# Kernel optimization log

Measured on AMD Instinct MI355X. Metric: run time of the kernel, lower is better.

## Reference

```python
import jax, jax.numpy as jnp
import numpy as np

THRESHOLD = 0.5
NEG_POS = 3
ALPHA = 1.0


def cxcy_to_xy(b):
    return jnp.concatenate([b[:, :2] - b[:, 2:] / 2, b[:, :2] + b[:, 2:] / 2], axis=-1)


def xy_to_cxcy(b):
    return jnp.concatenate([(b[:, :2] + b[:, 2:]) / 2, b[:, 2:] - b[:, :2]], axis=-1)


def encode_bboxes(cxcy, priors_cxcy):
    # standard SSD encoding with variances (0.1, 0.2)
    g_cxcy = (cxcy[:, :2] - priors_cxcy[:, :2]) / (priors_cxcy[:, 2:] / 10.0)
    g_wh = jnp.log(cxcy[:, 2:] / priors_cxcy[:, 2:]) * 5.0
    return jnp.concatenate([g_cxcy, g_wh], axis=-1)


def compute_iou(a, b):
    # a: [n,4] xyxy, b: [m,4] xyxy -> [n,m]
    lt = jnp.maximum(a[:, None, :2], b[None, :, :2])
    rb = jnp.minimum(a[:, None, 2:], b[None, :, 2:])
    wh = jnp.clip(rb - lt, 0.0)
    inter = wh[..., 0] * wh[..., 1]
    area_a = (a[:, 2] - a[:, 0]) * (a[:, 3] - a[:, 1])
    area_b = (b[:, 2] - b[:, 0]) * (b[:, 3] - b[:, 1])
    return inter / (area_a[:, None] + area_b[None, :] - inter)


def setup_inputs() -> dict:
    key = jax.random.key(0)
    k1, k2, k3, k4, k5, k6 = jax.random.split(key, 6)
    B, D, C, O = 128, 8732, 21, 16
    loc_pred = jax.random.normal(k1, (B, D, 4), dtype=jnp.float32)
    cls_pred = jax.random.normal(k2, (B, D, C), dtype=jnp.float32)
    # valid gt boxes: xmin<xmax, ymin<ymax
    p = jax.random.uniform(k3, (B, O, 4), dtype=jnp.float32)
    x1 = jnp.minimum(p[..., 0], p[..., 2])
    x2 = jnp.maximum(p[..., 0], p[..., 2]) + 1e-2
    y1 = jnp.minimum(p[..., 1], p[..., 3])
    y2 = jnp.maximum(p[..., 1], p[..., 3]) + 1e-2
    gt_boxes = jnp.stack([x1, y1, x2, y2], axis=-1)
    gt_labels = jax.random.randint(k4, (B, O), 1, C)
    # priors in cxcywh, w/h in (0.05, 0.5)
    cxy = jax.random.uniform(k5, (D, 2), dtype=jnp.float32)
    wh = jax.random.uniform(k6, (D, 2), dtype=jnp.float32) * 0.45 + 0.05
    default_boxes = jnp.concatenate([cxy, wh], axis=-1)
    return {"loc_pred": loc_pred, "cls_pred": cls_pred, "gt_boxes": gt_boxes,
            "gt_labels": gt_labels, "default_boxes": default_boxes}


def _match_and_losses(loc_pred, cls_pred, gt_boxes, gt_labels, default_boxes):
    B, D, C = cls_pred.shape
    O = gt_boxes.shape[1]
    db_xy = cxcy_to_xy(default_boxes)

    def match_one(boxes_i, labels_i):
        iou = compute_iou(boxes_i, db_xy)                 # [O, D]
        best_truth_overlap = iou.max(axis=0)              # [D]
        best_truth_idx = iou.argmax(axis=0)               # [D]
        best_default_idx = iou.argmax(axis=1)             # [O]
        best_truth_idx = best_truth_idx.at[best_default_idx].set(jnp.arange(O))
        best_truth_overlap = best_truth_overlap.at[best_default_idx].set(1.0)
        labels = labels_i[best_truth_idx]                 # [D]
        labels = jnp.where(best_truth_overlap < THRESHOLD, 0, labels)
        matched_xy = boxes_i[best_truth_idx]              # [D,4]
        loc = encode_bboxes(xy_to_cxcy(matched_xy), default_boxes)
        return loc, labels

    loc_t, conf_t = jax.vmap(match_one)(gt_boxes, gt_labels)  # [B,D,4], [B,D]
    loc_t = jax.lax.stop_gradient(loc_t)  # targets carry no grad (requires_grad=False)

    pos = conf_t > 0                                      # [B,D]
    n_positive = pos.sum(axis=1)                          # [B]
    n_pos_total = n_positive.sum()

    # SmoothL1 (beta=1), mean over positive elements (num_pos * 4)
    diff = loc_pred - loc_t
    ad = jnp.abs(diff)
    sl1 = jnp.where(ad < 1.0, 0.5 * diff * diff, ad - 0.5)
    loc_loss = (sl1 * pos[..., None]).sum() / (n_pos_total.astype(jnp.float32) * 4.0)

    # per-element cross entropy
    logp = jax.nn.log_softmax(cls_pred, axis=-1)          # [B,D,C]
    ce = -jnp.take_along_axis(logp, conf_t[..., None], axis=-1)[..., 0]  # [B,D]

    conf_pos_sum = (ce * pos).sum()
    neg_loss = jnp.where(pos, 0.0, ce)
    neg_sorted = -jnp.sort(-neg_loss, axis=1)             # descending per row
    ranks = jnp.arange(D)[None, :]
    hard = ranks < (NEG_POS * n_positive)[:, None]
    conf_neg_sum = (neg_sorted * hard).sum()
    conf_loss = (conf_neg_sum + conf_pos_sum) / n_pos_total.astype(jnp.float32)

    return ALPHA * loc_loss + conf_loss


def reference(loc_pred, cls_pred, gt_boxes, gt_labels, default_boxes):
    return _match_and_losses(loc_pred, cls_pred, gt_boxes, gt_labels, default_boxes)
```

## Files before the change

### kernel.cpp

```cpp
#include <hip/hip_runtime.h>

#define BB 128
#define DD 8732
#define OO 16
#define CC 21
#define CH 16
#define CHUNK 546
#define NBLK_D 35
#define NLB (BB * NBLK_D)
#define NV 35

typedef __attribute__((address_space(3))) unsigned int lds_u32;
typedef const __attribute__((address_space(1))) unsigned int glb_u32;

__device__ __forceinline__ float smoothl1(float d) {
    float ad = fabsf(d);
    return (ad < 1.0f) ? 0.5f * d * d : ad - 0.5f;
}

__global__ __launch_bounds__(256) void match_a(
    const float4* __restrict__ gt_boxes,
    const float4* __restrict__ db,
    unsigned long long* __restrict__ partial,
    unsigned* __restrict__ bpk,
    int* __restrict__ done_counter)
{
    const int b = blockIdx.y, ch = blockIdx.x, tid = threadIdx.x;
    if (b == 0 && ch == 0 && tid == 0) *done_counter = 0;

    __shared__ float s_ax1[OO], s_ay1[OO], s_ax2[OO], s_ay2[OO], s_area[OO];
    __shared__ unsigned long long s_keys[OO][257];

    if (tid < OO) {
        float4 g = gt_boxes[b * OO + tid];
        s_ax1[tid] = g.x; s_ay1[tid] = g.y; s_ax2[tid] = g.z; s_ay2[tid] = g.w;
        s_area[tid] = (g.z - g.x) * (g.w - g.y);
    }
    __syncthreads();

    unsigned long long key[OO];
    #pragma unroll
    for (int o = 0; o < OO; ++o) key[o] = 0ull;

    const int d0 = ch * CHUNK;
    const int dend = min(d0 + CHUNK, DD);
    for (int d = d0 + tid; d < dend; d += 256) {
        float4 p = db[d];
        float px1 = p.x - p.z * 0.5f, py1 = p.y - p.w * 0.5f;
        float px2 = p.x + p.z * 0.5f, py2 = p.y + p.w * 0.5f;
        float area_b = (px2 - px1) * (py2 - py1);
        unsigned dl = (unsigned)(DD - 1 - d);
        float best = -1.0f; int bi = 0;
        #pragma unroll
        for (int o = 0; o < OO; ++o) {
            float w = fmaxf(fminf(s_ax2[o], px2) - fmaxf(s_ax1[o], px1), 0.0f);
            float h = fmaxf(fminf(s_ay2[o], py2) - fmaxf(s_ay1[o], py1), 0.0f);
            float inter = w * h;
            float uni = s_area[o] + area_b - inter;
            float iou = inter * __builtin_amdgcn_rcpf(uni);
            unsigned long long kk = ((unsigned long long)__float_as_uint(iou) << 32) | dl;
            if (kk > key[o]) key[o] = kk;
            if (iou > best) { best = iou; bi = o; }
        }
        bpk[(size_t)b * DD + d] = (__float_as_uint(best) & 0xFFFFFF00u) | (unsigned)bi;
    }
    #pragma unroll
    for (int o = 0; o < OO; ++o) s_keys[o][tid] = key[o];
    __syncthreads();

    const int o = tid >> 4, j = tid & 15;
    unsigned long long mx = s_keys[o][j];
    #pragma unroll
    for (int m = 1; m < 16; ++m) {
        unsigned long long v = s_keys[o][j + 16 * m];
        if (v > mx) mx = v;
    }
    #pragma unroll
    for (int off = 8; off; off >>= 1) {
        unsigned long long v = __shfl_xor(mx, off, 16);
        if (v > mx) mx = v;
    }
    if (j == 0) partial[((size_t)b * OO + o) * CH + ch] = mx;
}

__global__ __launch_bounds__(256) void fused_main(
    const float4* __restrict__ loc_pred,
    const float*  __restrict__ cls,
    const float4* __restrict__ gt_boxes,
    const int*    __restrict__ gt_labels,
    const float4* __restrict__ db,
    const unsigned long long* __restrict__ partial,
    const unsigned* __restrict__ bpk,
    float* __restrict__ ce_neg,
    float* __restrict__ part_sl1,
    int*   __restrict__ part_np,
    float* __restrict__ part_ce)
{
    const int b = blockIdx.y, jb = blockIdx.x, tid = threadIdx.x;
    const int d = jb * 256 + tid;
    __shared__ float s_cls[256 * CC];
    __shared__ float s_ax1[OO], s_ay1[OO], s_ax2[OO], s_ay2[OO];
    __shared__ int   s_lab[OO], s_bdi[OO];
    __shared__ unsigned char s_ovr[256];
    __shared__ float s_f[8];
    __shared__ int   s_i[4];

    const int nrow = min(256, DD - jb * 256);
    const int nvec = nrow * CC / 4;
    const float4* src = (const float4*)(cls + ((size_t)b * DD + (size_t)jb * 256) * CC);
    if (nvec == 1344) {
        #pragma unroll
        for (int c = 0; c < 5; ++c) {
            int v = c * 256 + tid;
            __builtin_amdgcn_global_load_lds((glb_u32*)(src + v),
                                             (lds_u32*)&s_cls[v * 4], 16, 0, 0);
        }
        if (tid < 64) {
            int v = 5 * 256 + tid;
            __builtin_amdgcn_global_load_lds((glb_u32*)(src + v),
                                             (lds_u32*)&s_cls[v * 4], 16, 0, 0);
        }
    } else {
        for (int v = tid; v < nvec; v += 256)
            __builtin_amdgcn_global_load_lds((glb_u32*)(src + v),
                                             (lds_u32*)&s_cls[v * 4], 16, 0, 0);
    }

    s_ovr[tid] = 0xFF;
    if (tid < OO) {
        float4 g = gt_boxes[b * OO + tid];
        s_ax1[tid] = g.x; s_ay1[tid] = g.y; s_ax2[tid] = g.z; s_ay2[tid] = g.w;
        s_lab[tid] = gt_labels[b * OO + tid];
    }
    {
        unsigned long long k = partial[(size_t)b * (OO * CH) + tid];
        #pragma unroll
        for (int off = 8; off; off >>= 1) {
            unsigned long long v = __shfl_xor(k, off, 16);
            if (v > k) k = v;
        }
        if ((tid & 15) == 0) s_bdi[tid >> 4] = DD - 1 - (int)(k & 0xffffffffu);
    }
    const size_t gi = (size_t)b * DD + d;
    unsigned upk = 0u;
    if (d < DD) upk = bpk[gi];

    __syncthreads();

    if (tid == 0) {
        #pragma unroll
        for (int o = 0; o < OO; ++o) {
            int ds = s_bdi[o] - jb * 256;
            if (0 <= ds && ds < 256) s_ovr[ds] = (unsigned char)o;
        }
    }
    __syncthreads();

    float sl1 = 0.0f, cepos = 0.0f; int npos = 0;
    if (d < DD) {
        int bi = (int)(upk & 0xFFu);
        float best = __uint_as_float(upk & 0xFFFFFF00u);
        int ov = s_ovr[tid];
        if (ov != 0xFF) { bi = ov; best = 1.0f; }
        int lab = (best < 0.5f) ? 0 : s_lab[bi];

        float v[CC];
        #pragma unroll
        for (int c = 0; c < CC; ++c) v[c] = s_cls[tid * CC + c];
        float m = v[0];
        #pragma unroll
        for (int c = 1; c < CC; ++c) m = fmaxf(m, v[c]);
        float s = 0.0f;
        #pragma unroll
        for (int c = 0; c < CC; ++c) s += __expf(v[c] - m);
        float xl = s_cls[tid * CC + lab];
        float ce = m + __logf(s) - xl;

        if (lab > 0) {
            npos = 1; cepos = ce;
            float ax1 = s_ax1[bi], ay1 = s_ay1[bi], ax2 = s_ax2[bi], ay2 = s_ay2[bi];
            float cx = (ax1 + ax2) * 0.5f, cy = (ay1 + ay2) * 0.5f;
            float w = ax2 - ax1, h = ay2 - ay1;
            float4 p = db[d];
            float gx = (cx - p.x) / (p.z / 10.0f);
            float gy = (cy - p.y) / (p.w / 10.0f);
            float gw = __logf(w / p.z) * 5.0f;
            float gh = __logf(h / p.w) * 5.0f;
            float4 lp = loc_pred[gi];
            sl1 = smoothl1(lp.x - gx) + smoothl1(lp.y - gy)
                + smoothl1(lp.z - gw) + smoothl1(lp.w - gh);
        }
        ce_neg[gi] = (lab > 0) ? 0.0f : ce;
    }

    #pragma unroll
    for (int off = 32; off; off >>= 1) {
        sl1   += __shfl_xor(sl1, off);
        cepos += __shfl_xor(cepos, off);
        npos  += __shfl_xor(npos, off);
    }
    const int w = tid >> 6;
    if ((tid & 63) == 0) { s_f[w*2+0] = sl1; s_f[w*2+1] = cepos; s_i[w] = npos; }
    __syncthreads();
    if (tid == 0) {
        float sv = 0, cp = 0; int np = 0;
        #pragma unroll
        for (int q = 0; q < 4; ++q) { sv += s_f[q*2+0]; cp += s_f[q*2+1]; np += s_i[q]; }
        const int pi = b * NBLK_D + jb;
        part_sl1[pi] = sv;
        part_ce[pi]  = cp;
        part_np[pi]  = np;
    }
}

__global__ __launch_bounds__(256) void topk_final(
    const float* __restrict__ ce_neg,
    const int*   __restrict__ part_np,
    const float* __restrict__ part_sl1,
    const float* __restrict__ part_ce,
    float* __restrict__ conf_neg_part,
    int*   __restrict__ done_counter,
    float* __restrict__ out)
{
    const int b = blockIdx.x, tid = threadIdx.x;
    __shared__ int      hist[256];
    __shared__ unsigned s_pk[2];
    __shared__ float    s_f[12];
    __shared__ int      s_c[4];
    __shared__ int      s_last;

    int np = 0;
    #pragma unroll
    for (int jb = 0; jb < NBLK_D; ++jb) np += part_np[b * NBLK_D + jb];
    int k0 = 3 * np;
    if (k0 > DD) k0 = DD;

    float row = 0.0f;
    if (k0 > 0) {
        unsigned kx[NV];
        #pragma unroll
        for (int q = 0; q < NV; ++q) {
            int d = q * 256 + tid;
            float v = (d < DD) ? ce_neg[(size_t)b * DD + d] : 0.0f;
            unsigned u = __float_as_uint(v);
            kx[q] = u ^ ((unsigned)((int)u >> 31) | 0x80000000u);
        }

        unsigned prefix = 0u; int k = k0;
        #pragma unroll
        for (int p = 0; p < 4; ++p) {
            const int shift = 24 - 8 * p;
            hist[tid] = 0;
            __syncthreads();
            #pragma unroll
            for (int q = 0; q < NV; ++q) {
                if (p == 0 || ((kx[q] ^ prefix) >> (shift + 8)) == 0u)
                    atomicAdd(&hist[(kx[q] >> shift) & 255], 1);
            }
            __syncthreads();
            if (tid < 64) {
                int h0 = hist[255 - 4*tid], h1 = hist[254 - 4*tid],
                    h2 = hist[253 - 4*tid], h3 = hist[252 - 4*tid];
                int sl = h0 + h1 + h2 + h3;
                int run = sl;
                #pragma unroll
                for (int off = 1; off < 64; off <<= 1) {
                    int v = __shfl_up(run, off);
                    if (tid >= off) run += v;
                }
                int pre = run - sl;
                if (pre < k && k <= pre + sl) {
                    int hh[4] = {h0, h1, h2, h3};
                    int c = pre, byte = -1, knew = 0;
                    #pragma unroll
                    for (int j = 0; j < 4; ++j) {
                        if (byte < 0 && c + hh[j] >= k) { byte = 255 - 4*tid - j; knew = k - c; }
                        c += hh[j];
                    }
                    s_pk[0] = prefix | ((unsigned)byte << shift);
                    s_pk[1] = (unsigned)knew;
                }
            }
            __syncthreads();
            prefix = s_pk[0]; k = (int)s_pk[1];
        }

        unsigned vb = (prefix & 0x80000000u) ? (prefix ^ 0x80000000u) : ~prefix;
        float vk = __uint_as_float(vb);

        float ssum = 0.0f; int cgt = 0;
        #pragma unroll
        for (int q = 0; q < NV; ++q) {
            if (kx[q] > prefix) {
                unsigned u = (kx[q] & 0x80000000u) ? (kx[q] ^ 0x80000000u) : ~kx[q];
                ssum += __uint_as_float(u);
                ++cgt;
            }
        }
        #pragma unroll
        for (int off = 32; off; off >>= 1) { ssum += __shfl_xor(ssum, off); cgt += __shfl_xor(cgt, off); }
        if ((tid & 63) == 0) { s_f[tid >> 6] = ssum; s_c[tid >> 6] = cgt; }
        __syncthreads();
        row = s_f[0]+s_f[1]+s_f[2]+s_f[3]
            + (float)(k0 - (s_c[0]+s_c[1]+s_c[2]+s_c[3])) * vk;
    }

    if (tid == 0) {
        conf_neg_part[b] = row;
        __threadfence();
        int prev = atomicAdd(done_counter, 1);
        s_last = (prev == BB - 1) ? 1 : 0;
    }
    __syncthreads();
    if (s_last) {
        __threadfence();
        float loc = 0.0f, cp = 0.0f; int npt = 0;
        for (int i = tid; i < NLB; i += 256) {
            loc += part_sl1[i]; cp += part_ce[i]; npt += part_np[i];
        }
        float cn = (tid < BB) ? conf_neg_part[tid] : 0.0f;
        #pragma unroll
        for (int off = 32; off; off >>= 1) {
            loc += __shfl_xor(loc, off);
            cp  += __shfl_xor(cp, off);
            cn  += __shfl_xor(cn, off);
            npt += __shfl_xor(npt, off);
        }
        const int w = tid >> 6;
        if ((tid & 63) == 0) { s_f[w*3+0] = loc; s_f[w*3+1] = cp; s_f[w*3+2] = cn; s_c[w] = npt; }
        __syncthreads();
        if (tid == 0) {
            float L = 0, P = 0, N = 0; int T = 0;
            #pragma unroll
            for (int q = 0; q < 4; ++q) { L += s_f[q*3]; P += s_f[q*3+1]; N += s_f[q*3+2]; T += s_c[q]; }
            float npf = (float)T;
            out[0] = L / (npf * 4.0f) + (N + P) / npf;
        }
    }
}

extern "C" void kernel_launch(void* const* d_in, const int* in_sizes, int n_in,
                              void* d_out, int out_size, void* d_ws, size_t ws_size,
                              hipStream_t stream) {
    (void)in_sizes; (void)n_in; (void)out_size; (void)ws_size;
    const float4* loc_pred  = (const float4*)d_in[0];
    const float*  cls_pred  = (const float*)d_in[1];
    const float4* gt_boxes  = (const float4*)d_in[2];
    const int*    gt_labels = (const int*)d_in[3];
    const float4* db        = (const float4*)d_in[4];

    char* ws = (char*)d_ws;
    size_t off = 0;
    auto alloc = [&](size_t bytes) { char* p = ws + off; off = (off + bytes + 15) & ~(size_t)15; return p; };

    unsigned long long* partial = (unsigned long long*)alloc((size_t)BB * OO * CH * 8);
    float* ce_neg        = (float*)alloc((size_t)BB * DD * 4);
    unsigned* bpk        = (unsigned*)alloc((size_t)BB * DD * 4);
    float* part_sl1      = (float*)alloc((size_t)NLB * 4);
    int*   part_np       = (int*)alloc((size_t)NLB * 4);
    float* part_ce       = (float*)alloc((size_t)NLB * 4);
    float* conf_neg_part = (float*)alloc((size_t)BB * 4);
    int*   done_counter  = (int*)alloc(sizeof(int));

    match_a<<<dim3(CH, BB), 256, 0, stream>>>(gt_boxes, db, partial, bpk,
                                              done_counter);
    fused_main<<<dim3(NBLK_D, BB), 256, 0, stream>>>(loc_pred, cls_pred, gt_boxes,
                                                     gt_labels, db, partial, bpk,
                                                     ce_neg, part_sl1, part_np, part_ce);
    topk_final<<<BB, 256, 0, stream>>>(ce_neg, part_np, part_sl1, part_ce,
                                       conf_neg_part, done_counter, (float*)d_out);
}
```

Measured before the change: 67.19 us.

## Process four priors per thread with direct vectorized class-score loads

Measured after the change: 67.43 us. About the same (+0.4%).

```diff
diff --git a/kernel.cpp b/kernel.cpp
--- a/kernel.cpp
+++ b/kernel.cpp
@@ -6,12 +6,10 @@
 #define CC 21
 #define CH 16
 #define CHUNK 546
-#define NBLK_D 35
-#define NLB (BB * NBLK_D)
+#define NG4 2183
+#define NBLK_C 9
+#define NLB (BB * NBLK_C)
 #define NV 35
-
-typedef __attribute__((address_space(3))) unsigned int lds_u32;
-typedef const __attribute__((address_space(1))) unsigned int glb_u32;
 
 __device__ __forceinline__ float smoothl1(float d) {
     float ad = fabsf(d);
@@ -97,39 +95,16 @@
     float* __restrict__ part_ce)
 {
     const int b = blockIdx.y, jb = blockIdx.x, tid = threadIdx.x;
-    const int d = jb * 256 + tid;
-    __shared__ float s_cls[256 * CC];
+    const int g = jb * 256 + tid;
     __shared__ float s_ax1[OO], s_ay1[OO], s_ax2[OO], s_ay2[OO];
     __shared__ int   s_lab[OO], s_bdi[OO];
-    __shared__ unsigned char s_ovr[256];
+    __shared__ unsigned char s_ovr[1024];
     __shared__ float s_f[8];
     __shared__ int   s_i[4];
 
-    const int nrow = min(256, DD - jb * 256);
-    const int nvec = nrow * CC / 4;
-    const float4* src = (const float4*)(cls + ((size_t)b * DD + (size_t)jb * 256) * CC);
-    if (nvec == 1344) {
-        #pragma unroll
-        for (int c = 0; c < 5; ++c) {
-            int v = c * 256 + tid;
-            __builtin_amdgcn_global_load_lds((glb_u32*)(src + v),
-                                             (lds_u32*)&s_cls[v * 4], 16, 0, 0);
-        }
-        if (tid < 64) {
-            int v = 5 * 256 + tid;
-            __builtin_amdgcn_global_load_lds((glb_u32*)(src + v),
-                                             (lds_u32*)&s_cls[v * 4], 16, 0, 0);
-        }
-    } else {
-        for (int v = tid; v < nvec; v += 256)
-            __builtin_amdgcn_global_load_lds((glb_u32*)(src + v),
-                                             (lds_u32*)&s_cls[v * 4], 16, 0, 0);
-    }
-
-    s_ovr[tid] = 0xFF;
     if (tid < OO) {
-        float4 g = gt_boxes[b * OO + tid];
-        s_ax1[tid] = g.x; s_ay1[tid] = g.y; s_ax2[tid] = g.z; s_ay2[tid] = g.w;
+        float4 gg = gt_boxes[b * OO + tid];
+        s_ax1[tid] = gg.x; s_ay1[tid] = gg.y; s_ax2[tid] = gg.z; s_ay2[tid] = gg.w;
         s_lab[tid] = gt_labels[b * OO + tid];
     }
     {
@@ -141,56 +116,69 @@
         }
         if ((tid & 15) == 0) s_bdi[tid >> 4] = DD - 1 - (int)(k & 0xffffffffu);
     }
-    const size_t gi = (size_t)b * DD + d;
-    unsigned upk = 0u;
-    if (d < DD) upk = bpk[gi];
-
-    __syncthreads();
-
+    ((unsigned*)s_ovr)[tid] = 0xFFFFFFFFu;
+    __syncthreads();
     if (tid == 0) {
         #pragma unroll
         for (int o = 0; o < OO; ++o) {
-            int ds = s_bdi[o] - jb * 256;
-            if (0 <= ds && ds < 256) s_ovr[ds] = (unsigned char)o;
+            int ds = s_bdi[o] - jb * 1024;
+            if (0 <= ds && ds < 1024) s_ovr[ds] = (unsigned char)o;
         }
     }
     __syncthreads();
 
     float sl1 = 0.0f, cepos = 0.0f; int npos = 0;
-    if (d < DD) {
-        int bi = (int)(upk & 0xFFu);
-        float best = __uint_as_float(upk & 0xFFFFFF00u);
-        int ov = s_ovr[tid];
-        if (ov != 0xFF) { bi = ov; best = 1.0f; }
-        int lab = (best < 0.5f) ? 0 : s_lab[bi];
-
-        float v[CC];
-        #pragma unroll
-        for (int c = 0; c < CC; ++c) v[c] = s_cls[tid * CC + c];
-        float m = v[0];
-        #pragma unroll
-        for (int c = 1; c < CC; ++c) m = fmaxf(m, v[c]);
-        float s = 0.0f;
-        #pragma unroll
-        for (int c = 0; c < CC; ++c) s += __expf(v[c] - m);
-        float xl = s_cls[tid * CC + lab];
-        float ce = m + __logf(s) - xl;
-
-        if (lab > 0) {
-            npos = 1; cepos = ce;
-            float ax1 = s_ax1[bi], ay1 = s_ay1[bi], ax2 = s_ax2[bi], ay2 = s_ay2[bi];
-            float cx = (ax1 + ax2) * 0.5f, cy = (ay1 + ay2) * 0.5f;
-            float w = ax2 - ax1, h = ay2 - ay1;
-            float4 p = db[d];
-            float gx = (cx - p.x) / (p.z / 10.0f);
-            float gy = (cy - p.y) / (p.w / 10.0f);
-            float gw = __logf(w / p.z) * 5.0f;
-            float gh = __logf(h / p.w) * 5.0f;
-            float4 lp = loc_pred[gi];
-            sl1 = smoothl1(lp.x - gx) + smoothl1(lp.y - gy)
-                + smoothl1(lp.z - gw) + smoothl1(lp.w - gh);
-        }
-        ce_neg[gi] = (lab > 0) ? 0.0f : ce;
+    if (g < NG4) {
+        const int row0 = g * 4;
+        const size_t gi4 = (size_t)b * DD + row0;
+        float e[84];
+        const float4* src = (const float4*)(cls + gi4 * CC);
+        #pragma unroll
+        for (int jv = 0; jv < 21; ++jv) {
+            float4 q = src[jv];
+            e[4*jv+0] = q.x; e[4*jv+1] = q.y; e[4*jv+2] = q.z; e[4*jv+3] = q.w;
+        }
+        uint4 pk4 = *(const uint4*)(bpk + gi4);
+        unsigned pks[4] = {pk4.x, pk4.y, pk4.z, pk4.w};
+        float out[4];
+        #pragma unroll
+        for (int r = 0; r < 4; ++r) {
+            const int row = row0 + r;
+            unsigned upk = pks[r];
+            int bi = (int)(upk & 0xFFu);
+            float best = __uint_as_float(upk & 0xFFFFFF00u);
+            int ov = s_ovr[4 * tid + r];
+            if (ov != 0xFF) { bi = ov; best = 1.0f; }
+            int lab = (best < 0.5f) ? 0 : s_lab[bi];
+
+            float m = e[21*r];
+            #pragma unroll
+            for (int c = 1; c < CC; ++c) m = fmaxf(m, e[21*r + c]);
+            float s = 0.0f;
+            #pragma unroll
+            for (int c = 0; c < CC; ++c) s += __expf(e[21*r + c] - m);
+            float xl = (lab == 0) ? e[21*r] : cls[(gi4 + r) * CC + lab];
+            float ce = m + __logf(s) - xl;
+
+            if (lab > 0) {
+                npos += 1; cepos += ce;
+                float ax1 = s_ax1[bi], ay1 = s_ay1[bi], ax2 = s_ax2[bi], ay2 = s_ay2[bi];
+                float cx = (ax1 + ax2) * 0.5f, cy = (ay1 + ay2) * 0.5f;
+                float w = ax2 - ax1, h = ay2 - ay1;
+                float4 p = db[row];
+                float gx = (cx - p.x) / (p.z / 10.0f);
+                float gy = (cy - p.y) / (p.w / 10.0f);
+                float gw = __logf(w / p.z) * 5.0f;
+                float gh = __logf(h / p.w) * 5.0f;
+                float4 lp = loc_pred[gi4 + r];
+                sl1 += smoothl1(lp.x - gx) + smoothl1(lp.y - gy)
+                     + smoothl1(lp.z - gw) + smoothl1(lp.w - gh);
+                out[r] = 0.0f;
+            } else {
+                out[r] = ce;
+            }
+        }
+        *(float4*)(ce_neg + gi4) = make_float4(out[0], out[1], out[2], out[3]);
     }
 
     #pragma unroll
@@ -206,7 +194,7 @@
         float sv = 0, cp = 0; int np = 0;
         #pragma unroll
         for (int q = 0; q < 4; ++q) { sv += s_f[q*2+0]; cp += s_f[q*2+1]; np += s_i[q]; }
-        const int pi = b * NBLK_D + jb;
+        const int pi = b * NBLK_C + jb;
         part_sl1[pi] = sv;
         part_ce[pi]  = cp;
         part_np[pi]  = np;
@@ -231,7 +219,7 @@
 
     int np = 0;
     #pragma unroll
-    for (int jb = 0; jb < NBLK_D; ++jb) np += part_np[b * NBLK_D + jb];
+    for (int jb = 0; jb < NBLK_C; ++jb) np += part_np[b * NBLK_C + jb];
     int k0 = 3 * np;
     if (k0 > DD) k0 = DD;
 
@@ -364,7 +352,7 @@
 
     match_a<<<dim3(CH, BB), 256, 0, stream>>>(gt_boxes, db, partial, bpk,
                                               done_counter);
-    fused_main<<<dim3(NBLK_D, BB), 256, 0, stream>>>(loc_pred, cls_pred, gt_boxes,
+    fused_main<<<dim3(NBLK_C, BB), 256, 0, stream>>>(loc_pred, cls_pred, gt_boxes,
                                                      gt_labels, db, partial, bpk,
                                                      ce_neg, part_sl1, part_np, part_ce);
     topk_final<<<BB, 256, 0, stream>>>(ce_neg, part_np, part_sl1, part_ce,
```
